# Performance work log

Measured on AMD Instinct MI355X. Metric: run time of the kernel, lower is better.

The kernel has to match this reference:

```python
import jax, jax.numpy as jnp
import numpy as np

B, S, D = 4, 2048, 1024
H, DK = 16, 64
DOUT = 1024

def setup_inputs() -> dict:
    key = jax.random.key(0)
    ks = jax.random.split(key, 9)
    sc_in = 1.0 / np.sqrt(D)
    sc_cat = 1.0 / np.sqrt(H * DK)
    x = jax.random.normal(ks[0], (B, S, D), dtype=jnp.float32)
    Wq = jax.random.uniform(ks[1], (H, D, DK), jnp.float32, -sc_in, sc_in)
    bq = jax.random.uniform(ks[2], (H, DK), jnp.float32, -sc_in, sc_in)
    Wk = jax.random.uniform(ks[3], (H, D, DK), jnp.float32, -sc_in, sc_in)
    bk = jax.random.uniform(ks[4], (H, DK), jnp.float32, -sc_in, sc_in)
    Wv = jax.random.uniform(ks[5], (H, D, DK), jnp.float32, -sc_in, sc_in)
    bv = jax.random.uniform(ks[6], (H, DK), jnp.float32, -sc_in, sc_in)
    Wo = jax.random.uniform(ks[7], (H * DK, DOUT), jnp.float32, -sc_cat, sc_cat)
    bo = jax.random.uniform(ks[8], (DOUT,), jnp.float32, -sc_cat, sc_cat)
    return {"x": x, "Wq": Wq, "bq": bq, "Wk": Wk, "bk": bk, "Wv": Wv, "bv": bv, "Wo": Wo, "bo": bo}

def reference(x, Wq, bq, Wk, bk, Wv, bv, Wo, bo):
    # Per-head linear projections batched over heads: [B,S,D] x [H,D,K] -> [B,H,S,K]
    Q = jnp.einsum('bsd,hdk->bhsk', x, Wq) + bq[None, :, None, :]
    K = jnp.einsum('bsd,hdk->bhsk', x, Wk) + bk[None, :, None, :]
    V = jnp.einsum('bsd,hdk->bhsk', x, Wv) + bv[None, :, None, :]
    scale = 1.0 / jnp.sqrt(jnp.asarray(DK, dtype=x.dtype))
    scores = jnp.einsum('bhsk,bhtk->bhst', Q, K) * scale  # [B,H,S,S]
    attn = jax.nn.softmax(scores, axis=-1)
    heads = jnp.einsum('bhst,bhtk->bhsk', attn, V)  # [B,H,S,K]
    # concat heads along feature dim (head order = concat order)
    cat = jnp.transpose(heads, (0, 2, 1, 3)).reshape(x.shape[0], x.shape[1], H * DK)
    return cat @ Wo + bo
```

## Files before the change

kernel.cpp:

```cpp
#include <hip/hip_runtime.h>
#include <hip/hip_bf16.h>
#include <stdint.h>

typedef unsigned short u16;
typedef __attribute__((ext_vector_type(8))) short short8;
typedef __attribute__((ext_vector_type(4))) float f32x4;
typedef __attribute__((ext_vector_type(4))) unsigned short u16x4;

#define DEV static __device__ __forceinline__


DEV u16 f2bf(float f) {
  __hip_bfloat16 b = __float2bfloat16(f);
  return *(u16*)&b;
}

DEV void stage16(const u16* g, u16* l) {
  __builtin_amdgcn_global_load_lds((const __attribute__((address_space(1))) void*)g,
                                   (__attribute__((address_space(3))) void*)l, 16, 0, 0);
}

__global__ __launch_bounds__(256) void cvt_kernel(
    const float* __restrict__ x, const float* __restrict__ Wq,
    const float* __restrict__ Wk, const float* __restrict__ Wv,
    const float* __restrict__ Wo,
    u16* __restrict__ xb, u16* __restrict__ Wt, u16* __restrict__ Wot)
{
  int idx = blockIdx.x * 256 + threadIdx.x;
  if (idx < 1048576) {
    int i = idx * 8;
    f32x4 v0 = *(const f32x4*)&x[i];
    f32x4 v1 = *(const f32x4*)&x[i + 4];
    short8 o;
    o[0]=f2bf(v0[0]); o[1]=f2bf(v0[1]); o[2]=f2bf(v0[2]); o[3]=f2bf(v0[3]);
    o[4]=f2bf(v1[0]); o[5]=f2bf(v1[1]); o[6]=f2bf(v1[2]); o[7]=f2bf(v1[3]);
    *(short8*)&xb[i] = o;
  } else if (idx < 1835008) {
    int t = (idx - 1048576) * 4;
    int w = t >> 20; int r = t & 1048575; int n = r >> 10; int d0 = r & 1023;
    const float* W = (w == 0) ? Wq : (w == 1) ? Wk : Wv;
    int h = n >> 6, k = n & 63;
    u16x4 o;
    #pragma unroll
    for (int u = 0; u < 4; u++) o[u] = f2bf(W[(size_t)(h*1024 + d0 + u)*64 + k]);
    *(u16x4*)&Wt[t] = o;
  } else if (idx < 2097152) {
    int t = (idx - 1835008) * 4;
    int n = t >> 10, d0 = t & 1023;
    u16x4 o;
    #pragma unroll
    for (int u = 0; u < 4; u++) o[u] = f2bf(Wo[(size_t)(d0 + u)*1024 + n]);
    *(u16x4*)&Wot[t] = o;
  }
}

DEV void gemm_mainloop(const u16* __restrict__ A, const u16* __restrict__ Bt,
                       int m0, int n0, u16* As, u16* Bs, f32x4 acc[4][4])
{
  const int tid = threadIdx.x;
  const int lane = tid & 63, wid = tid >> 6;
  const int wr = wid >> 1, wc = wid & 1;
  const int qr = lane & 15, g = lane >> 4;
  const int c0 = wid * 2, rA = lane >> 2, cA = (lane & 3) * 8;

  #pragma unroll
  for (int i = 0; i < 4; i++)
    #pragma unroll
    for (int j = 0; j < 4; j++) acc[i][j] = (f32x4){0.f, 0.f, 0.f, 0.f};

  for (int kt = 0; kt < 1024; kt += 32) {
    #pragma unroll
    for (int q = 0; q < 2; q++) {
      const int c = c0 + q;
      stage16(A  + (size_t)(m0 + c*16 + rA)*1024 + kt + cA, &As[c*512]);
      stage16(Bt + (size_t)(n0 + c*16 + rA)*1024 + kt + cA, &Bs[c*512]);
    }
    __syncthreads();
    short8 af[4], bfr[4];
    #pragma unroll
    for (int i = 0; i < 4; i++) af[i]  = *(const short8*)&As[(wr*64 + i*16 + qr)*32 + g*8];
    #pragma unroll
    for (int j = 0; j < 4; j++) bfr[j] = *(const short8*)&Bs[(wc*64 + j*16 + qr)*32 + g*8];
    #pragma unroll
    for (int i = 0; i < 4; i++)
      #pragma unroll
      for (int j = 0; j < 4; j++)
        acc[i][j] = __builtin_amdgcn_mfma_f32_16x16x32_bf16(af[i], bfr[j], acc[i][j], 0, 0, 0);
    __syncthreads();
  }
}

__global__ __launch_bounds__(256) void qkv_gemm_kernel(
    const u16* __restrict__ A, const u16* __restrict__ WtAll,
    const float* __restrict__ bq, const float* __restrict__ bk, const float* __restrict__ bv,
    u16* __restrict__ Qo, u16* __restrict__ Ko, u16* __restrict__ Vo)
{
  __shared__ __align__(128) u16 As[4096];
  __shared__ __align__(128) u16 Bs[4096];
  const int lane = threadIdx.x & 63, wid = threadIdx.x >> 6;
  const int wr = wid >> 1, wc = wid & 1;
  const int qr = lane & 15, g = lane >> 4;
  const int m0 = blockIdx.y * 128, n0 = blockIdx.x * 128;
  const int mode = blockIdx.z;
  const u16* Bt = WtAll + (size_t)mode * 1048576;
  const float* bias = (mode == 0) ? bq : (mode == 1) ? bk : bv;
  const float osc = (mode == 0) ? 0.1803368867f : 1.0f;

  f32x4 acc[4][4];
  gemm_mainloop(A, Bt, m0, n0, As, Bs, acc);

  if (mode == 2) {
    #pragma unroll
    for (int i = 0; i < 4; i++) {
      const int mrow = m0 + wr*64 + i*16 + g*4;
      const int b = mrow >> 11, s = mrow & 2047;
      #pragma unroll
      for (int j = 0; j < 4; j++) {
        const int n = n0 + wc*64 + j*16 + qr;
        const float bz = bias[n];
        u16x4 v;
        #pragma unroll
        for (int r = 0; r < 4; r++) v[r] = f2bf(acc[i][j][r] + bz);
        *(u16x4*)&Vo[((size_t)(b*16 + (n >> 6))*64 + (n & 63))*2048 + s] = v;
      }
    }
  } else {
    u16* O = (mode == 0) ? Qo : Ko;
    #pragma unroll
    for (int i = 0; i < 4; i++) {
      const int mrow = m0 + wr*64 + i*16 + g*4;
      const int b = mrow >> 11, s = mrow & 2047;
      #pragma unroll
      for (int j = 0; j < 4; j++) {
        const int n = n0 + wc*64 + j*16 + qr;
        const float bz = bias[n];
        const size_t base = ((size_t)(b*16 + (n >> 6))*2048 + s)*64 + (n & 63);
        #pragma unroll
        for (int r = 0; r < 4; r++) O[base + (size_t)r*64] = f2bf((acc[i][j][r] + bz) * osc);
      }
    }
  }
}

__global__ __launch_bounds__(512, 2) void attn_kernel(
    const u16* __restrict__ Q, const u16* __restrict__ K,
    const u16* __restrict__ Vt, u16* __restrict__ cat)
{
  __shared__ __align__(16) u16 Ks[2][2048];
  __shared__ __align__(16) u16 Vs[2][2048];
  __shared__ __align__(16) u16 Pl[10240];
  const int lane = threadIdx.x & 63, w = threadIdx.x >> 6;
  const int bid = blockIdx.x;
  const int logical = (bid & 7) * 32 + (bid >> 3);
  const int bh = logical >> 2;
  const int xq = logical & 3;
  const int b = bh >> 4, h = bh & 15;
  const int q0 = xq * 512 + w * 64;
  const int qr = lane & 15, g = lane >> 4;
  u16* P0 = &Pl[(w*2 + 0)*640];
  u16* P1 = &Pl[(w*2 + 1)*640];

  const u16* Qb = Q  + (size_t)bh * 131072;
  const u16* Kb = K  + (size_t)bh * 131072;
  const u16* Vb = Vt + (size_t)bh * 131072;

  const int isK = (w < 4);
  const int krow = 8*w + (lane >> 3);
  const size_t ksrc = (size_t)krow*64 + (size_t)(((lane & 7) ^ (lane >> 3)) * 8);
  const int vw = w - 4, vrow = 16*vw + (lane >> 2);
  const size_t vsrc = (size_t)vrow*2048 + (size_t)(((lane & 3) ^ ((lane >> 3) & 3)) * 8);
  u16* kdst0 = &Ks[0][w*512];       u16* kdst1 = &Ks[1][w*512];
  u16* vdst0 = &Vs[0][vw*512];      u16* vdst1 = &Vs[1][vw*512];

  const int kro0 = qr*64        + ((g     ^ (qr & 7)) * 8);
  const int kro1 = qr*64        + (((4+g) ^ (qr & 7)) * 8);
  const int kro2 = (16+qr)*64   + ((g     ^ (qr & 7)) * 8);
  const int kro3 = (16+qr)*64   + (((4+g) ^ (qr & 7)) * 8);
  const int vro  = qr*32        + ((g ^ ((qr >> 1) & 3)) * 8);

  short8 qa[4], qb_[4];
  #pragma unroll
  for (int qs = 0; qs < 4; qs++) {
    qa[qs]  = *(const short8*)&Qb[(size_t)(q0 + qs*16 + qr)*64 + g*8];
    qb_[qs] = *(const short8*)&Qb[(size_t)(q0 + qs*16 + qr)*64 + 32 + g*8];
  }

  const short ONE = (short)0x3F80;
  const short8 ones = {ONE, ONE, ONE, ONE, ONE, ONE, ONE, ONE};

  f32x4 o[4][4];
  #pragma unroll
  for (int qs = 0; qs < 4; qs++)
    #pragma unroll
    for (int d = 0; d < 4; d++) o[qs][d] = (f32x4){0.f,0.f,0.f,0.f};
  f32x4 ol[4] = {{0.f,0.f,0.f,0.f},{0.f,0.f,0.f,0.f},{0.f,0.f,0.f,0.f},{0.f,0.f,0.f,0.f}};

  if (isK) stage16(Kb + ksrc, kdst0); else stage16(Vb + vsrc, vdst0);
  __syncthreads();

  for (int tt = 0; tt < 2048; tt += 32) {
    const int cur = (tt >> 5) & 1;
    const int tn = (tt + 32) & 2047;
    if (isK) stage16(Kb + (size_t)tn*64 + ksrc, cur ? kdst0 : kdst1);
    else     stage16(Vb + vsrc + tn,            cur ? vdst0 : vdst1);

    const u16* Kc = Ks[cur];
    const u16* Vc = Vs[cur];
    short8 kc0 = *(const short8*)&Kc[kro0];
    short8 kc1 = *(const short8*)&Kc[kro1];
    short8 kc2 = *(const short8*)&Kc[kro2];
    short8 kc3 = *(const short8*)&Kc[kro3];
    short8 vv0 = *(const short8*)&Vc[0*512 + vro];
    short8 vv1 = *(const short8*)&Vc[1*512 + vro];
    short8 vv2 = *(const short8*)&Vc[2*512 + vro];
    short8 vv3 = *(const short8*)&Vc[3*512 + vro];

    #pragma unroll
    for (int qs = 0; qs < 4; qs++) {
      f32x4 sl = {0.f,0.f,0.f,0.f}, sh = {0.f,0.f,0.f,0.f};
      sl = __builtin_amdgcn_mfma_f32_16x16x32_bf16(kc0, qa[qs],  sl, 0, 0, 0);
      sl = __builtin_amdgcn_mfma_f32_16x16x32_bf16(kc1, qb_[qs], sl, 0, 0, 0);
      sh = __builtin_amdgcn_mfma_f32_16x16x32_bf16(kc2, qa[qs],  sh, 0, 0, 0);
      sh = __builtin_amdgcn_mfma_f32_16x16x32_bf16(kc3, qb_[qs], sh, 0, 0, 0);
      u16x4 lo, hi;
      #pragma unroll
      for (int r = 0; r < 4; r++) {
        lo[r] = f2bf(__builtin_amdgcn_exp2f(sl[r]));
        hi[r] = f2bf(__builtin_amdgcn_exp2f(sh[r]));
      }
      u16* P = (qs & 1) ? P1 : P0;
      *(u16x4*)&P[qr*40 + g*4]      = lo;
      *(u16x4*)&P[qr*40 + 16 + g*4] = hi;
      short8 bp = *(const short8*)&P[qr*40 + g*8];
      ol[qs] = __builtin_amdgcn_mfma_f32_16x16x32_bf16(ones, bp, ol[qs], 0, 0, 0);
      o[qs][0] = __builtin_amdgcn_mfma_f32_16x16x32_bf16(vv0, bp, o[qs][0], 0, 0, 0);
      o[qs][1] = __builtin_amdgcn_mfma_f32_16x16x32_bf16(vv1, bp, o[qs][1], 0, 0, 0);
      o[qs][2] = __builtin_amdgcn_mfma_f32_16x16x32_bf16(vv2, bp, o[qs][2], 0, 0, 0);
      o[qs][3] = __builtin_amdgcn_mfma_f32_16x16x32_bf16(vv3, bp, o[qs][3], 0, 0, 0);
    }
    __syncthreads();
  }
  #pragma unroll
  for (int qs = 0; qs < 4; qs++) {
    const float inv = 1.0f / ol[qs][0];
    const size_t base = ((size_t)(b*2048 + q0 + qs*16 + qr))*1024 + h*64;
    #pragma unroll
    for (int d = 0; d < 4; d++) {
      u16x4 v;
      #pragma unroll
      for (int r = 0; r < 4; r++) v[r] = f2bf(o[qs][d][r] * inv);
      *(u16x4*)&cat[base + d*16 + g*4] = v;
    }
  }
}

__global__ __launch_bounds__(256) void out_gemm_kernel(
    const u16* __restrict__ A, const u16* __restrict__ Bt,
    const float* __restrict__ bias, float* __restrict__ out)
{
  __shared__ __align__(128) u16 As[4096];
  __shared__ __align__(128) u16 Bs[4096];
  const int lane = threadIdx.x & 63, wid = threadIdx.x >> 6;
  const int wr = wid >> 1, wc = wid & 1;
  const int qr = lane & 15, g = lane >> 4;
  const int m0 = blockIdx.y * 128, n0 = blockIdx.x * 128;

  f32x4 acc[4][4];
  gemm_mainloop(A, Bt, m0, n0, As, Bs, acc);

  #pragma unroll
  for (int i = 0; i < 4; i++) {
    const int mrow = m0 + wr*64 + i*16 + g*4;
    #pragma unroll
    for (int j = 0; j < 4; j++) {
      const int n = n0 + wc*64 + j*16 + qr;
      const float bz = bias[n];
      #pragma unroll
      for (int r = 0; r < 4; r++) out[(size_t)(mrow + r)*1024 + n] = acc[i][j][r] + bz;
    }
  }
}

extern "C" void kernel_launch(void* const* d_in, const int* in_sizes, int n_in,
                              void* d_out, int out_size, void* d_ws, size_t ws_size,
                              hipStream_t stream) {
  const float* x  = (const float*)d_in[0];
  const float* Wq = (const float*)d_in[1];
  const float* bq = (const float*)d_in[2];
  const float* Wk = (const float*)d_in[3];
  const float* bk = (const float*)d_in[4];
  const float* Wv = (const float*)d_in[5];
  const float* bv = (const float*)d_in[6];
  const float* Wo = (const float*)d_in[7];
  const float* bo = (const float*)d_in[8];
  float* out = (float*)d_out;
  char* ws = (char*)d_ws;

  u16* xb  = (u16*)(ws);
  u16* Wt  = (u16*)(ws + 16777216);
  u16* Wot = (u16*)(ws + 23068672);
  u16* Qb  = (u16*)(ws + 25165824);
  u16* Kb  = (u16*)(ws + 41943040);
  u16* Vt  = (u16*)(ws + 58720256);
  u16* cat = xb;

  cvt_kernel<<<8192, 256, 0, stream>>>(x, Wq, Wk, Wv, Wo, xb, Wt, Wot);
  qkv_gemm_kernel<<<dim3(8, 64, 3), 256, 0, stream>>>(xb, Wt, bq, bk, bv, Qb, Kb, Vt);
  attn_kernel<<<256, 512, 0, stream>>>(Qb, Kb, Vt, cat);
  out_gemm_kernel<<<dim3(8, 64), 256, 0, stream>>>(cat, Wot, bo, out);
}
```

Before: 202.1 us.

## Halve attention block size and double key tile to 64 per iteration

```diff
diff --git a/kernel.cpp b/kernel.cpp
--- a/kernel.cpp
+++ b/kernel.cpp
@@ -142,20 +142,20 @@
   }
 }
 
-__global__ __launch_bounds__(512, 2) void attn_kernel(
+__global__ __launch_bounds__(256, 2) void attn_kernel(
     const u16* __restrict__ Q, const u16* __restrict__ K,
     const u16* __restrict__ Vt, u16* __restrict__ cat)
 {
-  __shared__ __align__(16) u16 Ks[2][2048];
-  __shared__ __align__(16) u16 Vs[2][2048];
-  __shared__ __align__(16) u16 Pl[10240];
+  __shared__ __align__(16) u16 Ks[2][4096];
+  __shared__ __align__(16) u16 Vs[2][4096];
+  __shared__ __align__(16) u16 Pl[5120];
   const int lane = threadIdx.x & 63, w = threadIdx.x >> 6;
   const int bid = blockIdx.x;
-  const int logical = (bid & 7) * 32 + (bid >> 3);
-  const int bh = logical >> 2;
-  const int xq = logical & 3;
+  const int logical = (bid & 7) * 64 + (bid >> 3);
+  const int bh = logical >> 3;
+  const int xq = logical & 7;
   const int b = bh >> 4, h = bh & 15;
-  const int q0 = xq * 512 + w * 64;
+  const int q0 = xq * 256 + w * 64;
   const int qr = lane & 15, g = lane >> 4;
   u16* P0 = &Pl[(w*2 + 0)*640];
   u16* P1 = &Pl[(w*2 + 1)*640];
@@ -164,19 +164,13 @@
   const u16* Kb = K  + (size_t)bh * 131072;
   const u16* Vb = Vt + (size_t)bh * 131072;
 
-  const int isK = (w < 4);
-  const int krow = 8*w + (lane >> 3);
-  const size_t ksrc = (size_t)krow*64 + (size_t)(((lane & 7) ^ (lane >> 3)) * 8);
-  const int vw = w - 4, vrow = 16*vw + (lane >> 2);
-  const size_t vsrc = (size_t)vrow*2048 + (size_t)(((lane & 3) ^ ((lane >> 3) & 3)) * 8);
-  u16* kdst0 = &Ks[0][w*512];       u16* kdst1 = &Ks[1][w*512];
-  u16* vdst0 = &Vs[0][vw*512];      u16* vdst1 = &Vs[1][vw*512];
-
-  const int kro0 = qr*64        + ((g     ^ (qr & 7)) * 8);
-  const int kro1 = qr*64        + (((4+g) ^ (qr & 7)) * 8);
-  const int kro2 = (16+qr)*64   + ((g     ^ (qr & 7)) * 8);
-  const int kro3 = (16+qr)*64   + (((4+g) ^ (qr & 7)) * 8);
-  const int vro  = qr*32        + ((g ^ ((qr >> 1) & 3)) * 8);
+  const int srow0 = w*16 + (lane >> 3);
+  const int schunk = ((lane & 7) ^ (lane >> 3)) * 8;
+  const size_t ksrc0 = (size_t)srow0*64 + schunk;
+  const size_t ksrc1 = (size_t)(srow0+8)*64 + schunk;
+  const size_t vsrc0 = (size_t)srow0*2048 + schunk;
+  const size_t vsrc1 = (size_t)(srow0+8)*2048 + schunk;
+  const int ldst0 = w*1024, ldst1 = w*1024 + 512;
 
   short8 qa[4], qb_[4];
   #pragma unroll
@@ -195,48 +189,62 @@
     for (int d = 0; d < 4; d++) o[qs][d] = (f32x4){0.f,0.f,0.f,0.f};
   f32x4 ol[4] = {{0.f,0.f,0.f,0.f},{0.f,0.f,0.f,0.f},{0.f,0.f,0.f,0.f},{0.f,0.f,0.f,0.f}};
 
-  if (isK) stage16(Kb + ksrc, kdst0); else stage16(Vb + vsrc, vdst0);
+  stage16(Kb + ksrc0, &Ks[0][ldst0]);
+  stage16(Kb + ksrc1, &Ks[0][ldst1]);
+  stage16(Vb + vsrc0, &Vs[0][ldst0]);
+  stage16(Vb + vsrc1, &Vs[0][ldst1]);
   __syncthreads();
 
-  for (int tt = 0; tt < 2048; tt += 32) {
-    const int cur = (tt >> 5) & 1;
-    const int tn = (tt + 32) & 2047;
-    if (isK) stage16(Kb + (size_t)tn*64 + ksrc, cur ? kdst0 : kdst1);
-    else     stage16(Vb + vsrc + tn,            cur ? vdst0 : vdst1);
+  for (int tt = 0; tt < 2048; tt += 64) {
+    const int cur = (tt >> 6) & 1, nxt = cur ^ 1;
+    const int tn = (tt + 64) & 2047;
+    stage16(Kb + (size_t)tn*64 + ksrc0, &Ks[nxt][ldst0]);
+    stage16(Kb + (size_t)tn*64 + ksrc1, &Ks[nxt][ldst1]);
+    stage16(Vb + vsrc0 + tn,            &Vs[nxt][ldst0]);
+    stage16(Vb + vsrc1 + tn,            &Vs[nxt][ldst1]);
 
     const u16* Kc = Ks[cur];
     const u16* Vc = Vs[cur];
-    short8 kc0 = *(const short8*)&Kc[kro0];
-    short8 kc1 = *(const short8*)&Kc[kro1];
-    short8 kc2 = *(const short8*)&Kc[kro2];
-    short8 kc3 = *(const short8*)&Kc[kro3];
-    short8 vv0 = *(const short8*)&Vc[0*512 + vro];
-    short8 vv1 = *(const short8*)&Vc[1*512 + vro];
-    short8 vv2 = *(const short8*)&Vc[2*512 + vro];
-    short8 vv3 = *(const short8*)&Vc[3*512 + vro];
+    short8 kc[8];
+    #pragma unroll
+    for (int ts = 0; ts < 4; ts++)
+      #pragma unroll
+      for (int kk = 0; kk < 2; kk++)
+        kc[ts*2+kk] = *(const short8*)&Kc[(ts*16+qr)*64 + (((kk*4+g) ^ (qr&7))*8)];
+    short8 av[8];
+    #pragma unroll
+    for (int d = 0; d < 4; d++)
+      #pragma unroll
+      for (int th = 0; th < 2; th++)
+        av[d*2+th] = *(const short8*)&Vc[(d*16+qr)*64 + (((th*4+g) ^ (qr&7))*8)];
 
     #pragma unroll
     for (int qs = 0; qs < 4; qs++) {
-      f32x4 sl = {0.f,0.f,0.f,0.f}, sh = {0.f,0.f,0.f,0.f};
-      sl = __builtin_amdgcn_mfma_f32_16x16x32_bf16(kc0, qa[qs],  sl, 0, 0, 0);
-      sl = __builtin_amdgcn_mfma_f32_16x16x32_bf16(kc1, qb_[qs], sl, 0, 0, 0);
-      sh = __builtin_amdgcn_mfma_f32_16x16x32_bf16(kc2, qa[qs],  sh, 0, 0, 0);
-      sh = __builtin_amdgcn_mfma_f32_16x16x32_bf16(kc3, qb_[qs], sh, 0, 0, 0);
-      u16x4 lo, hi;
-      #pragma unroll
-      for (int r = 0; r < 4; r++) {
-        lo[r] = f2bf(__builtin_amdgcn_exp2f(sl[r]));
-        hi[r] = f2bf(__builtin_amdgcn_exp2f(sh[r]));
+      f32x4 s[4];
+      #pragma unroll
+      for (int ts = 0; ts < 4; ts++) {
+        s[ts] = (f32x4){0.f,0.f,0.f,0.f};
+        s[ts] = __builtin_amdgcn_mfma_f32_16x16x32_bf16(kc[ts*2],   qa[qs],  s[ts], 0, 0, 0);
+        s[ts] = __builtin_amdgcn_mfma_f32_16x16x32_bf16(kc[ts*2+1], qb_[qs], s[ts], 0, 0, 0);
       }
-      u16* P = (qs & 1) ? P1 : P0;
-      *(u16x4*)&P[qr*40 + g*4]      = lo;
-      *(u16x4*)&P[qr*40 + 16 + g*4] = hi;
-      short8 bp = *(const short8*)&P[qr*40 + g*8];
-      ol[qs] = __builtin_amdgcn_mfma_f32_16x16x32_bf16(ones, bp, ol[qs], 0, 0, 0);
-      o[qs][0] = __builtin_amdgcn_mfma_f32_16x16x32_bf16(vv0, bp, o[qs][0], 0, 0, 0);
-      o[qs][1] = __builtin_amdgcn_mfma_f32_16x16x32_bf16(vv1, bp, o[qs][1], 0, 0, 0);
-      o[qs][2] = __builtin_amdgcn_mfma_f32_16x16x32_bf16(vv2, bp, o[qs][2], 0, 0, 0);
-      o[qs][3] = __builtin_amdgcn_mfma_f32_16x16x32_bf16(vv3, bp, o[qs][3], 0, 0, 0);
+      u16x4 e[4];
+      #pragma unroll
+      for (int ts = 0; ts < 4; ts++)
+        #pragma unroll
+        for (int r = 0; r < 4; r++) e[ts][r] = f2bf(__builtin_amdgcn_exp2f(s[ts][r]));
+      *(u16x4*)&P0[qr*40 + g*4]      = e[0];
+      *(u16x4*)&P0[qr*40 + 16 + g*4] = e[1];
+      *(u16x4*)&P1[qr*40 + g*4]      = e[2];
+      *(u16x4*)&P1[qr*40 + 16 + g*4] = e[3];
+      short8 bp0 = *(const short8*)&P0[qr*40 + g*8];
+      short8 bp1 = *(const short8*)&P1[qr*40 + g*8];
+      ol[qs] = __builtin_amdgcn_mfma_f32_16x16x32_bf16(ones, bp0, ol[qs], 0, 0, 0);
+      ol[qs] = __builtin_amdgcn_mfma_f32_16x16x32_bf16(ones, bp1, ol[qs], 0, 0, 0);
+      #pragma unroll
+      for (int d = 0; d < 4; d++) {
+        o[qs][d] = __builtin_amdgcn_mfma_f32_16x16x32_bf16(av[d*2],   bp0, o[qs][d], 0, 0, 0);
+        o[qs][d] = __builtin_amdgcn_mfma_f32_16x16x32_bf16(av[d*2+1], bp1, o[qs][d], 0, 0, 0);
+      }
     }
     __syncthreads();
   }
@@ -306,6 +314,6 @@
 
   cvt_kernel<<<8192, 256, 0, stream>>>(x, Wq, Wk, Wv, Wo, xb, Wt, Wot);
   qkv_gemm_kernel<<<dim3(8, 64, 3), 256, 0, stream>>>(xb, Wt, bq, bk, bv, Qb, Kb, Vt);
-  attn_kernel<<<256, 512, 0, stream>>>(Qb, Kb, Vt, cat);
+  attn_kernel<<<512, 256, 0, stream>>>(Qb, Kb, Vt, cat);
   out_gemm_kernel<<<dim3(8, 64), 256, 0, stream>>>(cat, Wot, bo, out);
 }
```

Result: slower. 212.5 us (+5.1%).

## Triple-buffer attention K/V staging and remap GEMM blocks across XCDs

Applied to the files above, without the earlier changes.

```diff
diff --git a/kernel.cpp b/kernel.cpp
--- a/kernel.cpp
+++ b/kernel.cpp
@@ -100,8 +100,10 @@
   const int lane = threadIdx.x & 63, wid = threadIdx.x >> 6;
   const int wr = wid >> 1, wc = wid & 1;
   const int qr = lane & 15, g = lane >> 4;
-  const int m0 = blockIdx.y * 128, n0 = blockIdx.x * 128;
-  const int mode = blockIdx.z;
+  const int wg = (blockIdx.x & 7) * 192 + (blockIdx.x >> 3);
+  const int n0 = (wg & 7) * 128;
+  const int m0 = ((wg >> 3) & 63) * 128;
+  const int mode = wg >> 9;
   const u16* Bt = WtAll + (size_t)mode * 1048576;
   const float* bias = (mode == 0) ? bq : (mode == 1) ? bk : bv;
   const float osc = (mode == 0) ? 0.1803368867f : 1.0f;
@@ -146,8 +148,8 @@
     const u16* __restrict__ Q, const u16* __restrict__ K,
     const u16* __restrict__ Vt, u16* __restrict__ cat)
 {
-  __shared__ __align__(16) u16 Ks[2][2048];
-  __shared__ __align__(16) u16 Vs[2][2048];
+  __shared__ __align__(16) u16 Ks[3][2048];
+  __shared__ __align__(16) u16 Vs[3][2048];
   __shared__ __align__(16) u16 Pl[10240];
   const int lane = threadIdx.x & 63, w = threadIdx.x >> 6;
   const int bid = blockIdx.x;
@@ -169,8 +171,7 @@
   const size_t ksrc = (size_t)krow*64 + (size_t)(((lane & 7) ^ (lane >> 3)) * 8);
   const int vw = w - 4, vrow = 16*vw + (lane >> 2);
   const size_t vsrc = (size_t)vrow*2048 + (size_t)(((lane & 3) ^ ((lane >> 3) & 3)) * 8);
-  u16* kdst0 = &Ks[0][w*512];       u16* kdst1 = &Ks[1][w*512];
-  u16* vdst0 = &Vs[0][vw*512];      u16* vdst1 = &Vs[1][vw*512];
+  const int koff = w*512, voff = vw*512;
 
   const int kro0 = qr*64        + ((g     ^ (qr & 7)) * 8);
   const int kro1 = qr*64        + (((4+g) ^ (qr & 7)) * 8);
@@ -195,25 +196,32 @@
     for (int d = 0; d < 4; d++) o[qs][d] = (f32x4){0.f,0.f,0.f,0.f};
   f32x4 ol[4] = {{0.f,0.f,0.f,0.f},{0.f,0.f,0.f,0.f},{0.f,0.f,0.f,0.f},{0.f,0.f,0.f,0.f}};
 
-  if (isK) stage16(Kb + ksrc, kdst0); else stage16(Vb + vsrc, vdst0);
-  __syncthreads();
+  if (isK) {
+    stage16(Kb + ksrc,            &Ks[0][koff]);
+    stage16(Kb + 2048 + ksrc,     &Ks[1][koff]);
+  } else {
+    stage16(Vb + vsrc,            &Vs[0][voff]);
+    stage16(Vb + vsrc + 32,       &Vs[1][voff]);
+  }
+
+  const u16 *kc_cur = &Ks[0][0], *kc_nx1 = &Ks[1][0], *kc_stg = &Ks[2][0];
+  const u16 *vc_cur = &Vs[0][0], *vc_nx1 = &Vs[1][0], *vc_stg = &Vs[2][0];
 
   for (int tt = 0; tt < 2048; tt += 32) {
-    const int cur = (tt >> 5) & 1;
-    const int tn = (tt + 32) & 2047;
-    if (isK) stage16(Kb + (size_t)tn*64 + ksrc, cur ? kdst0 : kdst1);
-    else     stage16(Vb + vsrc + tn,            cur ? vdst0 : vdst1);
-
-    const u16* Kc = Ks[cur];
-    const u16* Vc = Vs[cur];
-    short8 kc0 = *(const short8*)&Kc[kro0];
-    short8 kc1 = *(const short8*)&Kc[kro1];
-    short8 kc2 = *(const short8*)&Kc[kro2];
-    short8 kc3 = *(const short8*)&Kc[kro3];
-    short8 vv0 = *(const short8*)&Vc[0*512 + vro];
-    short8 vv1 = *(const short8*)&Vc[1*512 + vro];
-    short8 vv2 = *(const short8*)&Vc[2*512 + vro];
-    short8 vv3 = *(const short8*)&Vc[3*512 + vro];
+    asm volatile("s_waitcnt vmcnt(1)" ::: "memory");
+    __builtin_amdgcn_s_barrier();
+    const int tn = (tt + 64) & 2047;
+    if (isK) stage16(Kb + (size_t)tn*64 + ksrc, (u16*)kc_stg + koff);
+    else     stage16(Vb + vsrc + tn,            (u16*)vc_stg + voff);
+
+    short8 kc0 = *(const short8*)&kc_cur[kro0];
+    short8 kc1 = *(const short8*)&kc_cur[kro1];
+    short8 kc2 = *(const short8*)&kc_cur[kro2];
+    short8 kc3 = *(const short8*)&kc_cur[kro3];
+    short8 vv0 = *(const short8*)&vc_cur[0*512 + vro];
+    short8 vv1 = *(const short8*)&vc_cur[1*512 + vro];
+    short8 vv2 = *(const short8*)&vc_cur[2*512 + vro];
+    short8 vv3 = *(const short8*)&vc_cur[3*512 + vro];
 
     #pragma unroll
     for (int qs = 0; qs < 4; qs++) {
@@ -238,7 +246,8 @@
       o[qs][2] = __builtin_amdgcn_mfma_f32_16x16x32_bf16(vv2, bp, o[qs][2], 0, 0, 0);
       o[qs][3] = __builtin_amdgcn_mfma_f32_16x16x32_bf16(vv3, bp, o[qs][3], 0, 0, 0);
     }
-    __syncthreads();
+    const u16* t0 = kc_cur; kc_cur = kc_nx1; kc_nx1 = kc_stg; kc_stg = t0;
+    const u16* t1 = vc_cur; vc_cur = vc_nx1; vc_nx1 = vc_stg; vc_stg = t1;
   }
   #pragma unroll
   for (int qs = 0; qs < 4; qs++) {
@@ -263,7 +272,9 @@
   const int lane = threadIdx.x & 63, wid = threadIdx.x >> 6;
   const int wr = wid >> 1, wc = wid & 1;
   const int qr = lane & 15, g = lane >> 4;
-  const int m0 = blockIdx.y * 128, n0 = blockIdx.x * 128;
+  const int wg = (blockIdx.x & 7) * 64 + (blockIdx.x >> 3);
+  const int n0 = (wg & 7) * 128;
+  const int m0 = (wg >> 3) * 128;
 
   f32x4 acc[4][4];
   gemm_mainloop(A, Bt, m0, n0, As, Bs, acc);
@@ -305,7 +316,7 @@
   u16* cat = xb;
 
   cvt_kernel<<<8192, 256, 0, stream>>>(x, Wq, Wk, Wv, Wo, xb, Wt, Wot);
-  qkv_gemm_kernel<<<dim3(8, 64, 3), 256, 0, stream>>>(xb, Wt, bq, bk, bv, Qb, Kb, Vt);
+  qkv_gemm_kernel<<<1536, 256, 0, stream>>>(xb, Wt, bq, bk, bv, Qb, Kb, Vt);
   attn_kernel<<<256, 512, 0, stream>>>(Qb, Kb, Vt, cat);
-  out_gemm_kernel<<<dim3(8, 64), 256, 0, stream>>>(cat, Wot, bo, out);
-}
+  out_gemm_kernel<<<512, 256, 0, stream>>>(cat, Wot, bo, out);
+}
```

Result: faster. 195.0 us (-3.5%).
